# Optimization experiments

Measured on AMD Instinct MI355X. Metric: run time of the kernel, lower is better.

## Reference

```python
import jax, jax.numpy as jnp
import numpy as np

IN_F = 512
OUT_F = 512
TREES = 50
DEPTH = 10  # levels above leaves; 2^DEPTH leaves per tree


def _build_forest(T, D):
    """Forest of T perfect binary trees. Nodes laid out level-by-level (leaves first).
    Returns node_order [N], adjacency [E,2] (parent, child; children consecutive,
    left then right, edges sorted by parent), edge_order [E]."""
    per = 2 ** (D + 1) - 1
    no = np.zeros(per, np.int64)
    adj_parts, eo_parts = [], []
    start, prev = 0, None
    for l in range(D + 1):
        n_l = 2 ** (D - l)
        idx = np.arange(start, start + n_l, dtype=np.int64)
        no[idx] = l
        if l > 0:
            parents = np.repeat(idx, 2)          # each parent twice
            adj_parts.append(np.stack([parents, prev], 1))  # prev = 2*n_l children, pairs consecutive
            eo_parts.append(np.full(2 * n_l, l, np.int64))
        prev, start = idx, start + n_l
    adj = np.concatenate(adj_parts, 0)
    eo = np.concatenate(eo_parts, 0)
    offs = np.arange(T, dtype=np.int64) * per
    node_order = np.tile(no, T)
    adjacency = (adj[None] + offs[:, None, None]).reshape(-1, 2)
    edge_order = np.tile(eo, T)
    return node_order, adjacency, edge_order


def setup_inputs() -> dict:
    key = jax.random.key(0)
    ks = jax.random.split(key, 8)
    no, adj, eo = _build_forest(TREES, DEPTH)
    N = no.shape[0]
    s_in = 1.0 / np.sqrt(IN_F).astype(np.float32)
    s_h = 1.0 / np.sqrt(OUT_F).astype(np.float32)
    return {
        "features": jax.random.normal(ks[0], (N, IN_F), jnp.float32),
        "node_order": jnp.asarray(no),
        "adjacency_list": jnp.asarray(adj),
        "edge_order": jnp.asarray(eo),
        "W_iou_w": jax.random.normal(ks[1], (3 * OUT_F, IN_F), jnp.float32) * s_in,
        "W_iou_b": jax.random.normal(ks[2], (3 * OUT_F,), jnp.float32) * s_in,
        "U_iou_l": jax.random.normal(ks[3], (3 * OUT_F, OUT_F), jnp.float32) * s_h,
        "U_iou_r": jax.random.normal(ks[4], (3 * OUT_F, OUT_F), jnp.float32) * s_h,
        "W_f_w": jax.random.normal(ks[5], (OUT_F, IN_F), jnp.float32) * s_in,
        "W_f_b": jax.random.normal(ks[6], (OUT_F,), jnp.float32) * s_in,
        "U_f_l": jax.random.normal(ks[7], (OUT_F, OUT_F), jnp.float32) * s_h,
        "U_f_r": jax.random.normal(jax.random.fold_in(key, 99), (OUT_F, OUT_F), jnp.float32) * s_h,
    }


def reference(features, node_order, adjacency_list, edge_order,
              W_iou_w, W_iou_b, U_iou_l, U_iou_r, W_f_w, W_f_b, U_f_l, U_f_r):
    # Tree topology is static integer data: hoist it to numpy so per-level index
    # sets are concrete (the original torch code host-syncs the same way).
    no = np.asarray(node_order)
    ao = np.asarray(adjacency_list)
    eo = np.asarray(edge_order)
    N, H = features.shape[0], W_f_w.shape[0]
    h = jnp.zeros((N, H), features.dtype)
    c = jnp.zeros((N, H), features.dtype)
    for l in range(int(no.max()) + 1):
        nodes = jnp.asarray(np.nonzero(no == l)[0])   # parents at this level, sorted
        x = features[nodes]                            # [P, F]
        if l == 0:
            iou = x @ W_iou_w.T + W_iou_b
            i, o, u = jnp.split(iou, 3, axis=1)
            c_new = jax.nn.sigmoid(i) * jnp.tanh(u)
        else:
            e = ao[eo == l]                            # [2P, 2]; children consecutive per parent
            p_rep = jnp.asarray(e[:, 0])               # parent repeated per child
            children = jnp.asarray(e[:, 1])
            ch = h[children]                           # [2P, H]
            cc = c[children]                           # [2P, H]
            iou = (x @ W_iou_w.T + W_iou_b
                   + ch[0::2] @ U_iou_l.T              # left child h
                   + ch[1::2] @ U_iou_r.T)             # right child h
            i, o, u = jnp.split(iou, 3, axis=1)
            wf = features[p_rep] @ W_f_w.T + W_f_b     # [2P, H]
            f_l = jax.nn.sigmoid(wf + ch @ U_f_l.T)
            f_r = jax.nn.sigmoid(wf + ch @ U_f_r.T)
            fc = (f_l + f_r) * cc                      # [2P, H]
            c_new = jax.nn.sigmoid(i) * jnp.tanh(u) + fc.reshape(-1, 2, H).sum(1)
        h_new = jax.nn.sigmoid(o) * jnp.tanh(c_new)
        c = c.at[nodes].set(c_new)
        h = h.at[nodes].set(h_new)
    return h, c
```

## Files before the change

### kernel.cpp

```cpp
#include <hip/hip_runtime.h>
#include <hip/hip_bf16.h>

#define TREES_ 50
#define PER_ 2047
#define NN_ (TREES_ * PER_)
#define NINT_ (TREES_ * 1023)
#define NLEAF_ (TREES_ * 1024)

typedef __attribute__((ext_vector_type(8))) short s8v;
typedef __attribute__((ext_vector_type(4))) float f4v;

__device__ __forceinline__ unsigned short f2bf(float f) {
  union { float f; unsigned u; } v; v.f = f;
  unsigned r = v.u + 0x7FFFu + ((v.u >> 16) & 1u);
  return (unsigned short)(r >> 16);
}
__device__ __forceinline__ float bf2f(unsigned short s) {
  union { unsigned u; float f; } v; v.u = ((unsigned)s) << 16;
  return v.f;
}
__device__ __forceinline__ float sigm(float x) { return 1.f / (1.f + __expf(-x)); }
__device__ __forceinline__ float tanh_s(float x) {
  float ax = fabsf(x);
  float e = __expf(2.f * ax);
  float t = 1.f - 2.f / (e + 1.f);
  return copysignf(t, x);
}
__device__ __forceinline__ f4v fz4() { f4v z; z[0]=0.f; z[1]=0.f; z[2]=0.f; z[3]=0.f; return z; }

#if defined(__has_builtin)
#if __has_builtin(__builtin_amdgcn_global_load_lds)
#define HAS_GLD 1
#endif
#endif
__device__ __forceinline__ void gld16(const void* g, void* l) {
#ifdef HAS_GLD
  __builtin_amdgcn_global_load_lds(
      (const __attribute__((address_space(1))) unsigned int*)g,
      (__attribute__((address_space(3))) unsigned int*)l, 16, 0, 0);
#else
  *(s8v*)l = *(const s8v*)g;
#endif
}

__device__ __forceinline__ int xcd_swz(int bid, int nwg) {
  int q = nwg >> 3, r = nwg & 7, x = bid & 7, pos = bid >> 3;
  int base = (x < r) ? x * (q + 1) : r * (q + 1) + (x - r) * q;
  return base + pos;
}

#define LDS_BYTE(row, c16) ((row) * 128 + (((c16) ^ ((row) & 7)) << 4))

#define MFMA_STEP(Ap, Bp)                                                     \
  _Pragma("unroll") for (int kk = 0; kk < 2; ++kk) {                          \
    s8v af[4], bf_[4];                                                        \
    _Pragma("unroll") for (int i = 0; i < 4; ++i) {                           \
      int R = wr * 64 + i * 16 + lr;                                          \
      af[i] = *(const s8v*)((const char*)(Ap) + LDS_BYTE(R, kk * 4 + lg));    \
    }                                                                         \
    _Pragma("unroll") for (int j = 0; j < 4; ++j) {                           \
      int R = wc * 64 + j * 16 + lr;                                          \
      bf_[j] = *(const s8v*)((const char*)(Bp) + LDS_BYTE(R, kk * 4 + lg));   \
    }                                                                         \
    _Pragma("unroll") for (int i = 0; i < 4; ++i)                             \
      _Pragma("unroll") for (int j = 0; j < 4; ++j)                           \
        acc[i][j] = __builtin_amdgcn_mfma_f32_16x16x32_bf16(af[i], bf_[j],    \
                                                            acc[i][j], 0, 0, 0); \
  }

#define VMCNT8() asm volatile("s_waitcnt vmcnt(8)" ::: "memory")
#define VMCNT0() asm volatile("s_waitcnt vmcnt(0)" ::: "memory")
#define LGKM0()  asm volatile("s_waitcnt lgkmcnt(0)" ::: "memory")
#define SBAR()   __builtin_amdgcn_s_barrier()
#define SCHEDB() __builtin_amdgcn_sched_barrier(0)

#define PIPELINE(STAGEM, NT)                                       \
  STAGEM(0, 0)                                                     \
  STAGEM(1, 64)                                                    \
  {                                                                \
    int cur = 0;                                                   \
    for (int t = 0; t < (NT) - 1; ++t) {                           \
      VMCNT8(); SBAR();                                            \
      __builtin_amdgcn_s_setprio(1);                               \
      MFMA_STEP(AsB + cur * 8192, BsB + cur * 8192)                \
      __builtin_amdgcn_s_setprio(0);                               \
      LGKM0(); SCHEDB(); SBAR();                                   \
      if (t + 2 < (NT)) { STAGEM(cur, (t + 2) * 64) }              \
      cur ^= 1;                                                    \
    }                                                              \
    VMCNT0(); SBAR();                                              \
    MFMA_STEP(AsB + cur * 8192, BsB + cur * 8192)                  \
  }

__global__ __launch_bounds__(256) void feat2bf(const float* __restrict__ feat,
                                               unsigned short* __restrict__ FB) {
  long long i = (long long)blockIdx.x * 256 + threadIdx.x;
  if (i >= (long long)NN_ * 64) return;
  const float* src = feat + i * 8;
  float4 f0 = *(const float4*)src;
  float4 f1 = *(const float4*)(src + 4);
  s8v v;
  v[0] = (short)f2bf(f0.x); v[1] = (short)f2bf(f0.y);
  v[2] = (short)f2bf(f0.z); v[3] = (short)f2bf(f0.w);
  v[4] = (short)f2bf(f1.x); v[5] = (short)f2bf(f1.y);
  v[6] = (short)f2bf(f1.z); v[7] = (short)f2bf(f1.w);
  *(s8v*)(FB + i * 8) = v;
}

__global__ __launch_bounds__(256) void prep_weights(
    const float* __restrict__ Wiou, const float* __restrict__ Ul,
    const float* __restrict__ Ur,  const float* __restrict__ Wf,
    const float* __restrict__ Ufl, const float* __restrict__ Ufr,
    unsigned short* __restrict__ UCAT2, unsigned short* __restrict__ UFLR,
    unsigned short* __restrict__ WFB) {
  int i = blockIdx.x * 256 + threadIdx.x;
  if (i < 1536 * 1536) {
    int r = i / 1536, c = i - r * 1536;
    float v = (c < 512) ? Ul[r * 512 + c]
            : (c < 1024) ? Ur[r * 512 + (c - 512)]
                         : Wiou[r * 512 + (c - 1024)];
    UCAT2[i] = f2bf(v);
  }
  if (i < 1024 * 512) {
    int r = i >> 9, k = i & 511;
    int c = r >> 1, s = r & 1;
    UFLR[i] = f2bf(s ? Ufr[c * 512 + k] : Ufl[c * 512 + k]);
  }
  if (i < 512 * 512) WFB[i] = f2bf(Wf[i]);
}

__global__ __launch_bounds__(256) void pre_mm(
    const unsigned short* __restrict__ FB, const unsigned short* __restrict__ WFB,
    const unsigned short* __restrict__ UCAT2,
    const float* __restrict__ bfb, const float* __restrict__ biou,
    unsigned short* __restrict__ WF, unsigned short* __restrict__ LIOU,
    int nwgW, int nwgL) {
  __shared__ __align__(16) unsigned short AsB[2 * 128 * 64];
  __shared__ __align__(16) unsigned short BsB[2 * 128 * 64];
  const int tid = threadIdx.x;
  const int wid = tid >> 6, lane = tid & 63;
  const int wr = wid >> 1, wc = wid & 1;
  const int lr = lane & 15, lg = lane >> 4;
  f4v acc[4][4];
#pragma unroll
  for (int i = 0; i < 4; ++i)
#pragma unroll
    for (int j = 0; j < 4; ++j) acc[i][j] = fz4();

  const unsigned short* aA[4]; const unsigned short* aB[4];
  int tm, tn;
  const bool isW = (int)blockIdx.x < nwgW;
  if (isW) {
    const int swz = xcd_swz(blockIdx.x, nwgW);
    tn = swz & 3; tm = swz >> 2;
#pragma unroll
    for (int L = 0; L < 4; ++L) {
      int q = L * 256 + tid;
      int row = q >> 3, c16g = (q & 7) ^ (row & 7);
      int m = tm * 128 + row; if (m >= NINT_) m = NINT_ - 1;
      unsigned t = (unsigned)m / 1023u;
      int node = (int)t * 2047 + 1024 + (m - (int)t * 1023);
      aA[L] = FB + (size_t)node * 512 + c16g * 8;
      int n = tn * 128 + row;
      aB[L] = WFB + (size_t)n * 512 + c16g * 8;
    }
  } else {
    const int swz = xcd_swz((int)blockIdx.x - nwgW, nwgL);
    tn = swz % 12; tm = swz / 12;
#pragma unroll
    for (int L = 0; L < 4; ++L) {
      int q = L * 256 + tid;
      int row = q >> 3, c16g = (q & 7) ^ (row & 7);
      int m = tm * 128 + row;
      int node = (m >> 10) * 2047 + (m & 1023);
      aA[L] = FB + (size_t)node * 512 + c16g * 8;
      int n = tn * 128 + row;
      aB[L] = UCAT2 + (size_t)n * 1536 + 1024 + c16g * 8;
    }
  }
#define STAGE_P(bb, kofs)                                         \
  _Pragma("unroll") for (int L = 0; L < 4; ++L) {                 \
    int q = L * 256 + tid;                                        \
    gld16(aA[L] + (kofs), AsB + (bb) * 8192 + q * 8);             \
    gld16(aB[L] + (kofs), BsB + (bb) * 8192 + q * 8);             \
  }
  PIPELINE(STAGE_P, 8)

  if (isW) {
#pragma unroll
    for (int i = 0; i < 4; ++i)
#pragma unroll
      for (int j = 0; j < 4; ++j) {
        int n = tn * 128 + wc * 64 + j * 16 + lr;
        float bias = bfb[n];
#pragma unroll
        for (int r = 0; r < 4; ++r) {
          int m = tm * 128 + wr * 64 + i * 16 + lg * 4 + r;
          if (m < NINT_) WF[(size_t)m * 512 + n] = f2bf(acc[i][j][r] + bias);
        }
      }
  } else {
#pragma unroll
    for (int i = 0; i < 4; ++i)
#pragma unroll
      for (int j = 0; j < 4; ++j) {
        int n = tn * 128 + wc * 64 + j * 16 + lr;
        float bias = biou[n];
#pragma unroll
        for (int r = 0; r < 4; ++r) {
          int m = tm * 128 + wr * 64 + i * 16 + lg * 4 + r;
          LIOU[(size_t)m * 1536 + n] = f2bf(acc[i][j][r] + bias);
        }
      }
  }
}

__global__ __launch_bounds__(256) void leaf_ew(
    const unsigned short* __restrict__ LIOU,
    float* __restrict__ h_out, float* __restrict__ c_out,
    unsigned short* __restrict__ HB) {
  int idx = blockIdx.x * 256 + threadIdx.x;
  int r = idx >> 7;
  int c4 = (idx & 127) << 2;
  int g = (r >> 10) * 2047 + (r & 1023);
  const unsigned short* pr = LIOU + (size_t)r * 1536;
  ushort4 iv = *(const ushort4*)(pr + c4);
  ushort4 ov = *(const ushort4*)(pr + 512 + c4);
  ushort4 uv = *(const ushort4*)(pr + 1024 + c4);
  float4 hv, cv; ushort4 hb;
  float cc, hh;
  cc = sigm(bf2f(iv.x)) * tanh_s(bf2f(uv.x)); hh = sigm(bf2f(ov.x)) * tanh_s(cc);
  cv.x = cc; hv.x = hh; hb.x = f2bf(hh);
  cc = sigm(bf2f(iv.y)) * tanh_s(bf2f(uv.y)); hh = sigm(bf2f(ov.y)) * tanh_s(cc);
  cv.y = cc; hv.y = hh; hb.y = f2bf(hh);
  cc = sigm(bf2f(iv.z)) * tanh_s(bf2f(uv.z)); hh = sigm(bf2f(ov.z)) * tanh_s(cc);
  cv.z = cc; hv.z = hh; hb.z = f2bf(hh);
  cc = sigm(bf2f(iv.w)) * tanh_s(bf2f(uv.w)); hh = sigm(bf2f(ov.w)) * tanh_s(cc);
  cv.w = cc; hv.w = hh; hb.w = f2bf(hh);
  *(float4*)(h_out + (size_t)g * 512 + c4) = hv;
  *(float4*)(c_out + (size_t)g * 512 + c4) = cv;
  *(ushort4*)(HB + (size_t)g * 512 + c4) = hb;
}

__global__ __launch_bounds__(256) void lvl_gemm(
    const unsigned short* __restrict__ HB, const unsigned short* __restrict__ FB,
    const unsigned short* __restrict__ UFLR, const unsigned short* __restrict__ UCAT2,
    const unsigned short* __restrict__ WF, const float* __restrict__ biou,
    const float* __restrict__ c_out, float* __restrict__ h_out,
    unsigned short* __restrict__ IOU,
    int P, int shift, int start_l, int start_lm1, int nwg1, int nwg2) {
  __shared__ __align__(16) unsigned short AsB[2 * 128 * 64];
  __shared__ __align__(16) unsigned short BsB[2 * 128 * 64];
  const int tid = threadIdx.x;
  const int wid = tid >> 6, lane = tid & 63;
  const int wr = wid >> 1, wc = wid & 1;
  const int lr = lane & 15, lg = lane >> 4;
  const int pmask = (1 << shift) - 1;
  f4v acc[4][4];
#pragma unroll
  for (int i = 0; i < 4; ++i)
#pragma unroll
    for (int j = 0; j < 4; ++j) acc[i][j] = fz4();

  if ((int)blockIdx.x < nwg1) {
    const int swz = xcd_swz(blockIdx.x, nwg1);
    const int tn = swz & 7, tm = swz >> 3;
    const int M2 = 2 * P;
    const int cmask = (2 << shift) - 1;
    const unsigned short* aA[4]; const unsigned short* aB[4];
#pragma unroll
    for (int L = 0; L < 4; ++L) {
      int q = L * 256 + tid;
      int row = q >> 3, c16g = (q & 7) ^ (row & 7);
      int jg = tm * 128 + row; if (jg >= M2) jg = M2 - 1;
      int t = jg >> (shift + 1), idx = jg & cmask;
      aA[L] = HB + (size_t)(t * PER_ + start_lm1 + idx) * 512 + c16g * 8;
      int n = tn * 128 + row;
      aB[L] = UFLR + (size_t)n * 512 + c16g * 8;
    }
#define STAGE_G1(bb, kofs)                                        \
  _Pragma("unroll") for (int L = 0; L < 4; ++L) {                 \
    int q = L * 256 + tid;                                        \
    gld16(aA[L] + (kofs), AsB + (bb) * 8192 + q * 8);             \
    gld16(aB[L] + (kofs), BsB + (bb) * 8192 + q * 8);             \
  }
    PIPELINE(STAGE_G1, 8)

    const int soff = start_l - 1024;
#pragma unroll
    for (int i = 0; i < 4; ++i) {
      int mbase = tm * 128 + wr * 64 + i * 16;
#pragma unroll
      for (int j = 0; j < 4; ++j) {
        int nn = tn * 128 + wc * 64 + j * 16 + lr;
        int hcol = nn >> 1;
        float fc[4];
#pragma unroll
        for (int r = 0; r < 4; ++r) {
          int m = mbase + lg * 4 + r;
          int mm = (m < M2) ? m : 0;
          int pidx = mm >> 1;
          int t = pidx >> shift, k = pidx & pmask;
          float wf = bf2f(WF[(size_t)(t * 1023 + soff + k) * 512 + hcol]);
          float sv = sigm(wf + acc[i][j][r]);
          float spair = sv + __shfl_xor(sv, 1, 64);
          float cc = 0.f;
          if ((lr & 1) == 0)
            cc = c_out[(size_t)(t * PER_ + start_lm1 + (mm & cmask)) * 512 + hcol];
          fc[r] = spair * cc;
        }
        if ((lr & 1) == 0) {
          int p0 = (mbase >> 1) + lg * 2;
          if (p0 < P) {
            int t0 = p0 >> shift, k0p = p0 & pmask;
            h_out[(size_t)(t0 * PER_ + start_l + k0p) * 512 + hcol] = fc[0] + fc[1];
          }
          int p1 = (mbase >> 1) + lg * 2 + 1;
          if (p1 < P) {
            int t1 = p1 >> shift, k1p = p1 & pmask;
            h_out[(size_t)(t1 * PER_ + start_l + k1p) * 512 + hcol] = fc[2] + fc[3];
          }
        }
      }
    }
  } else {
    const int swz = xcd_swz((int)blockIdx.x - nwg1, nwg2);
    const int tn = swz % 12, tm = swz / 12;
    const unsigned short* aHB[4]; const unsigned short* aFB[4];
    const unsigned short* aB[4];
#pragma unroll
    for (int L = 0; L < 4; ++L) {
      int q = L * 256 + tid;
      int row = q >> 3, c16g = (q & 7) ^ (row & 7);
      int p = tm * 128 + row; if (p >= P) p = P - 1;
      int t = p >> shift, kp = p & pmask;
      aHB[L] = HB + (size_t)(t * PER_ + start_lm1) * 512 + (size_t)kp * 1024 + c16g * 8;
      aFB[L] = FB + (size_t)(t * PER_ + start_l + kp) * 512 + c16g * 8 - 1024;
      int n = tn * 128 + row;
      aB[L] = UCAT2 + (size_t)n * 1536 + c16g * 8;
    }
#define STAGE_G2(bb, kofs)                                                    \
  _Pragma("unroll") for (int L = 0; L < 4; ++L) {                             \
    int q = L * 256 + tid;                                                    \
    const unsigned short* srcA =                                              \
        ((kofs) < 1024) ? aHB[L] + (kofs) : aFB[L] + (kofs);                  \
    gld16(srcA, AsB + (bb) * 8192 + q * 8);                                   \
    gld16(aB[L] + (kofs), BsB + (bb) * 8192 + q * 8);                         \
  }
    PIPELINE(STAGE_G2, 24)
#pragma unroll
    for (int i = 0; i < 4; ++i)
#pragma unroll
      for (int j = 0; j < 4; ++j) {
        int n = tn * 128 + wc * 64 + j * 16 + lr;
        float bias = biou[n];
#pragma unroll
        for (int r = 0; r < 4; ++r) {
          int m = tm * 128 + wr * 64 + i * 16 + lg * 4 + r;
          if (m < P) IOU[(size_t)m * 1536 + n] = f2bf(acc[i][j][r] + bias);
        }
      }
  }
}

__global__ __launch_bounds__(256) void g3_kernel(
    const unsigned short* __restrict__ IOU,
    float* __restrict__ h_out, float* __restrict__ c_out,
    unsigned short* __restrict__ HB, int P, int shift, int start_l) {
  int idx = blockIdx.x * 256 + threadIdx.x;
  int p = idx >> 7;
  if (p >= P) return;
  int c4 = (idx & 127) << 2;
  int t = p >> shift, k = p & ((1 << shift) - 1);
  size_t pg = (size_t)(t * PER_ + start_l + k);
  const unsigned short* ir = IOU + (size_t)p * 1536;
  ushort4 iv = *(const ushort4*)(ir + c4);
  ushort4 ov = *(const ushort4*)(ir + 512 + c4);
  ushort4 uv = *(const ushort4*)(ir + 1024 + c4);
  float4 fcs = *(const float4*)(h_out + pg * 512 + c4);
  float4 hv, cv; ushort4 hb;
  float cc, hh;
  cc = sigm(bf2f(iv.x)) * tanh_s(bf2f(uv.x)) + fcs.x; hh = sigm(bf2f(ov.x)) * tanh_s(cc);
  cv.x = cc; hv.x = hh; hb.x = f2bf(hh);
  cc = sigm(bf2f(iv.y)) * tanh_s(bf2f(uv.y)) + fcs.y; hh = sigm(bf2f(ov.y)) * tanh_s(cc);
  cv.y = cc; hv.y = hh; hb.y = f2bf(hh);
  cc = sigm(bf2f(iv.z)) * tanh_s(bf2f(uv.z)) + fcs.z; hh = sigm(bf2f(ov.z)) * tanh_s(cc);
  cv.z = cc; hv.z = hh; hb.z = f2bf(hh);
  cc = sigm(bf2f(iv.w)) * tanh_s(bf2f(uv.w)) + fcs.w; hh = sigm(bf2f(ov.w)) * tanh_s(cc);
  cv.w = cc; hv.w = hh; hb.w = f2bf(hh);
  *(float4*)(h_out + pg * 512 + c4) = hv;
  *(float4*)(c_out + pg * 512 + c4) = cv;
  *(ushort4*)(HB + pg * 512 + c4) = hb;
}

__global__ void fill_sentinel(float* out, int n) {
  int i = blockIdx.x * 256 + threadIdx.x;
  if (i < n) out[i] = 12345.0f;
}

extern "C" void kernel_launch(void* const* d_in, const int* in_sizes, int n_in,
                              void* d_out, int out_size, void* d_ws, size_t ws_size,
                              hipStream_t stream) {
  (void)in_sizes; (void)n_in; (void)out_size;
  const float* feat = (const float*)d_in[0];
  const float* Wiou = (const float*)d_in[4];
  const float* biou = (const float*)d_in[5];
  const float* Ul   = (const float*)d_in[6];
  const float* Ur   = (const float*)d_in[7];
  const float* Wf   = (const float*)d_in[8];
  const float* bfb  = (const float*)d_in[9];
  const float* Ufl  = (const float*)d_in[10];
  const float* Ufr  = (const float*)d_in[11];
  float* h_out = (float*)d_out;
  float* c_out = h_out + (size_t)NN_ * 512;

  const size_t OFF_HB   = 0;
  const size_t SZ_HB    = (size_t)NN_ * 512 * 2;
  const size_t OFF_FB   = OFF_HB + SZ_HB;
  const size_t SZ_FB    = (size_t)NN_ * 512 * 2;
  const size_t OFF_WFm  = OFF_FB + SZ_FB;
  const size_t SZ_WF    = (size_t)NINT_ * 512 * 2;
  const size_t OFF_UC2  = OFF_WFm + SZ_WF;
  const size_t SZ_UC2   = 1536 * 1536 * 2;
  const size_t OFF_UFLR = OFF_UC2 + SZ_UC2;
  const size_t SZ_UFLR  = 1024 * 512 * 2;
  const size_t OFF_WFB  = OFF_UFLR + SZ_UFLR;
  const size_t SZ_WFB   = 512 * 512 * 2;
  const size_t OFF_LIOU = OFF_WFB + SZ_WFB;
  const size_t SZ_LIOU  = (size_t)NLEAF_ * 1536 * 2;
  const size_t NEEDED   = OFF_LIOU + SZ_LIOU;

  if (ws_size < NEEDED) {
    int n = 2 * NN_ * 512;
    fill_sentinel<<<(n + 255) / 256, 256, 0, stream>>>((float*)d_out, n);
    return;
  }

  char* ws = (char*)d_ws;
  unsigned short* HB    = (unsigned short*)(ws + OFF_HB);
  unsigned short* FB    = (unsigned short*)(ws + OFF_FB);
  unsigned short* WF    = (unsigned short*)(ws + OFF_WFm);
  unsigned short* UCAT2 = (unsigned short*)(ws + OFF_UC2);
  unsigned short* UFLR  = (unsigned short*)(ws + OFF_UFLR);
  unsigned short* WFB   = (unsigned short*)(ws + OFF_WFB);
  unsigned short* LIOU  = (unsigned short*)(ws + OFF_LIOU);
  unsigned short* IOU   = (unsigned short*)(ws + OFF_LIOU);

  prep_weights<<<9216, 256, 0, stream>>>(Wiou, Ul, Ur, Wf, Ufl, Ufr,
                                         UCAT2, UFLR, WFB);
  feat2bf<<<(NN_ * 64 + 255) / 256, 256, 0, stream>>>(feat, FB);
  {
    int nwgW = ((NINT_ + 127) / 128) * 4;
    int nwgL = (NLEAF_ / 128) * 12;
    pre_mm<<<nwgW + nwgL, 256, 0, stream>>>(FB, WFB, UCAT2, bfb, biou,
                                            WF, LIOU, nwgW, nwgL);
  }
  leaf_ew<<<(NLEAF_ * 128) / 256, 256, 0, stream>>>(LIOU, h_out, c_out, HB);

  for (int l = 1; l <= 10; ++l) {
    int shift = 10 - l;
    int P = TREES_ << shift;
    int start_l   = 2048 - (1 << (11 - l));
    int start_lm1 = 2048 - (1 << (12 - l));
    int nwg1 = ((2 * P + 127) / 128) * 8;
    int nwg2 = ((P + 127) / 128) * 12;
    lvl_gemm<<<nwg1 + nwg2, 256, 0, stream>>>(HB, FB, UFLR, UCAT2, WF, biou,
                                              c_out, h_out, IOU,
                                              P, shift, start_l, start_lm1,
                                              nwg1, nwg2);
    int g3b = (P * 128 + 255) / 256;
    g3_kernel<<<g3b, 256, 0, stream>>>(IOU, h_out, c_out, HB, P, shift, start_l);
  }
}
```

Measured before the change: 1.460 ms.

## Split fused GEMM kernels and retile IOU GEMM with 256-wide triple-buffered tiles

Splits the merged pre-GEMM into separate wf_gemm and pre_mm launches, and splits the per-level fused kernel into g1_kernel (forget gates) and g2_kernel (IOU). g2 now uses 512-thread blocks with 128x256 tiles and a three-stage LDS ring with a wait of vmcnt(6), aiming for more B-tile reuse and deeper load/compute overlap. The cost is extra launches per level, and the forget and IOU GEMMs, which were independent, now run one after the other instead of concurrently.

Result: slower. 1.788 ms (+22.5%).

```diff
diff --git a/kernel.cpp b/kernel.cpp
--- a/kernel.cpp
+++ b/kernel.cpp
@@ -69,6 +69,7 @@
   }
 
 #define VMCNT8() asm volatile("s_waitcnt vmcnt(8)" ::: "memory")
+#define VMCNT6() asm volatile("s_waitcnt vmcnt(6)" ::: "memory")
 #define VMCNT0() asm volatile("s_waitcnt vmcnt(0)" ::: "memory")
 #define LGKM0()  asm volatile("s_waitcnt lgkmcnt(0)" ::: "memory")
 #define SBAR()   __builtin_amdgcn_s_barrier()
@@ -129,12 +130,60 @@
   if (i < 512 * 512) WFB[i] = f2bf(Wf[i]);
 }
 
+__global__ __launch_bounds__(256) void wf_gemm(
+    const unsigned short* __restrict__ FB, const unsigned short* __restrict__ WFB,
+    const float* __restrict__ bfb, unsigned short* __restrict__ WF, int nwg) {
+  __shared__ __align__(16) unsigned short AsB[2 * 128 * 64];
+  __shared__ __align__(16) unsigned short BsB[2 * 128 * 64];
+  const int tid = threadIdx.x;
+  const int swz = xcd_swz(blockIdx.x, nwg);
+  const int tn = swz & 3, tm = swz >> 2;
+  const int wid = tid >> 6, lane = tid & 63;
+  const int wr = wid >> 1, wc = wid & 1;
+  const int lr = lane & 15, lg = lane >> 4;
+  const unsigned short* aA[4]; const unsigned short* aB[4];
+#pragma unroll
+  for (int L = 0; L < 4; ++L) {
+    int q = L * 256 + tid;
+    int row = q >> 3, c16g = (q & 7) ^ (row & 7);
+    int m = tm * 128 + row; if (m >= NINT_) m = NINT_ - 1;
+    int t = (int)((unsigned)m / 1023u);
+    int node = t * 2047 + 1024 + (m - t * 1023);
+    aA[L] = FB + (size_t)node * 512 + c16g * 8;
+    int n = tn * 128 + row;
+    aB[L] = WFB + (size_t)n * 512 + c16g * 8;
+  }
+  f4v acc[4][4];
+#pragma unroll
+  for (int i = 0; i < 4; ++i)
+#pragma unroll
+    for (int j = 0; j < 4; ++j) acc[i][j] = fz4();
+#define STAGE_W(bb, kofs)                                         \
+  _Pragma("unroll") for (int L = 0; L < 4; ++L) {                 \
+    int q = L * 256 + tid;                                        \
+    gld16(aA[L] + (kofs), AsB + (bb) * 8192 + q * 8);             \
+    gld16(aB[L] + (kofs), BsB + (bb) * 8192 + q * 8);             \
+  }
+  PIPELINE(STAGE_W, 8)
+#pragma unroll
+  for (int i = 0; i < 4; ++i)
+#pragma unroll
+    for (int j = 0; j < 4; ++j) {
+      int n = tn * 128 + wc * 64 + j * 16 + lr;
+      float bias = bfb[n];
+#pragma unroll
+      for (int r = 0; r < 4; ++r) {
+        int m = tm * 128 + wr * 64 + i * 16 + lg * 4 + r;
+        if (m < NINT_) WF[(size_t)m * 512 + n] = f2bf(acc[i][j][r] + bias);
+      }
+    }
+}
+
 __global__ __launch_bounds__(256) void pre_mm(
-    const unsigned short* __restrict__ FB, const unsigned short* __restrict__ WFB,
+    const unsigned short* __restrict__ FB,
     const unsigned short* __restrict__ UCAT2,
-    const float* __restrict__ bfb, const float* __restrict__ biou,
-    unsigned short* __restrict__ WF, unsigned short* __restrict__ LIOU,
-    int nwgW, int nwgL) {
+    const float* __restrict__ biou,
+    unsigned short* __restrict__ LIOU, int nwg) {
   __shared__ __align__(16) unsigned short AsB[2 * 128 * 64];
   __shared__ __align__(16) unsigned short BsB[2 * 128 * 64];
   const int tid = threadIdx.x;
@@ -146,37 +195,18 @@
   for (int i = 0; i < 4; ++i)
 #pragma unroll
     for (int j = 0; j < 4; ++j) acc[i][j] = fz4();
-
   const unsigned short* aA[4]; const unsigned short* aB[4];
-  int tm, tn;
-  const bool isW = (int)blockIdx.x < nwgW;
-  if (isW) {
-    const int swz = xcd_swz(blockIdx.x, nwgW);
-    tn = swz & 3; tm = swz >> 2;
-#pragma unroll
-    for (int L = 0; L < 4; ++L) {
-      int q = L * 256 + tid;
-      int row = q >> 3, c16g = (q & 7) ^ (row & 7);
-      int m = tm * 128 + row; if (m >= NINT_) m = NINT_ - 1;
-      unsigned t = (unsigned)m / 1023u;
-      int node = (int)t * 2047 + 1024 + (m - (int)t * 1023);
-      aA[L] = FB + (size_t)node * 512 + c16g * 8;
-      int n = tn * 128 + row;
-      aB[L] = WFB + (size_t)n * 512 + c16g * 8;
-    }
-  } else {
-    const int swz = xcd_swz((int)blockIdx.x - nwgW, nwgL);
-    tn = swz % 12; tm = swz / 12;
-#pragma unroll
-    for (int L = 0; L < 4; ++L) {
-      int q = L * 256 + tid;
-      int row = q >> 3, c16g = (q & 7) ^ (row & 7);
-      int m = tm * 128 + row;
-      int node = (m >> 10) * 2047 + (m & 1023);
-      aA[L] = FB + (size_t)node * 512 + c16g * 8;
-      int n = tn * 128 + row;
-      aB[L] = UCAT2 + (size_t)n * 1536 + 1024 + c16g * 8;
-    }
+  const int swz = xcd_swz(blockIdx.x, nwg);
+  const int tn = swz % 12, tm = swz / 12;
+#pragma unroll
+  for (int L = 0; L < 4; ++L) {
+    int q = L * 256 + tid;
+    int row = q >> 3, c16g = (q & 7) ^ (row & 7);
+    int m = tm * 128 + row;
+    int node = (m >> 10) * 2047 + (m & 1023);
+    aA[L] = FB + (size_t)node * 512 + c16g * 8;
+    int n = tn * 128 + row;
+    aB[L] = UCAT2 + (size_t)n * 1536 + 1024 + c16g * 8;
   }
 #define STAGE_P(bb, kofs)                                         \
   _Pragma("unroll") for (int L = 0; L < 4; ++L) {                 \
@@ -185,34 +215,18 @@
     gld16(aB[L] + (kofs), BsB + (bb) * 8192 + q * 8);             \
   }
   PIPELINE(STAGE_P, 8)
-
-  if (isW) {
-#pragma unroll
-    for (int i = 0; i < 4; ++i)
-#pragma unroll
-      for (int j = 0; j < 4; ++j) {
-        int n = tn * 128 + wc * 64 + j * 16 + lr;
-        float bias = bfb[n];
-#pragma unroll
-        for (int r = 0; r < 4; ++r) {
-          int m = tm * 128 + wr * 64 + i * 16 + lg * 4 + r;
-          if (m < NINT_) WF[(size_t)m * 512 + n] = f2bf(acc[i][j][r] + bias);
-        }
+#pragma unroll
+  for (int i = 0; i < 4; ++i)
+#pragma unroll
+    for (int j = 0; j < 4; ++j) {
+      int n = tn * 128 + wc * 64 + j * 16 + lr;
+      float bias = biou[n];
+#pragma unroll
+      for (int r = 0; r < 4; ++r) {
+        int m = tm * 128 + wr * 64 + i * 16 + lg * 4 + r;
+        LIOU[(size_t)m * 1536 + n] = f2bf(acc[i][j][r] + bias);
       }
-  } else {
-#pragma unroll
-    for (int i = 0; i < 4; ++i)
-#pragma unroll
-      for (int j = 0; j < 4; ++j) {
-        int n = tn * 128 + wc * 64 + j * 16 + lr;
-        float bias = biou[n];
-#pragma unroll
-        for (int r = 0; r < 4; ++r) {
-          int m = tm * 128 + wr * 64 + i * 16 + lg * 4 + r;
-          LIOU[(size_t)m * 1536 + n] = f2bf(acc[i][j][r] + bias);
-        }
-      }
-  }
+    }
 }
 
 __global__ __launch_bounds__(256) void leaf_ew(
@@ -242,13 +256,11 @@
   *(ushort4*)(HB + (size_t)g * 512 + c4) = hb;
 }
 
-__global__ __launch_bounds__(256) void lvl_gemm(
-    const unsigned short* __restrict__ HB, const unsigned short* __restrict__ FB,
-    const unsigned short* __restrict__ UFLR, const unsigned short* __restrict__ UCAT2,
-    const unsigned short* __restrict__ WF, const float* __restrict__ biou,
-    const float* __restrict__ c_out, float* __restrict__ h_out,
-    unsigned short* __restrict__ IOU,
-    int P, int shift, int start_l, int start_lm1, int nwg1, int nwg2) {
+__global__ __launch_bounds__(256) void g1_kernel(
+    const unsigned short* __restrict__ HB, const unsigned short* __restrict__ UFLR,
+    const unsigned short* __restrict__ WF, const float* __restrict__ c_out,
+    float* __restrict__ h_out,
+    int P, int shift, int start_l, int start_lm1, int nwg) {
   __shared__ __align__(16) unsigned short AsB[2 * 128 * 64];
   __shared__ __align__(16) unsigned short BsB[2 * 128 * 64];
   const int tid = threadIdx.x;
@@ -256,111 +268,168 @@
   const int wr = wid >> 1, wc = wid & 1;
   const int lr = lane & 15, lg = lane >> 4;
   const int pmask = (1 << shift) - 1;
+  const int swz = xcd_swz(blockIdx.x, nwg);
+  const int tn = swz & 7, tm = swz >> 3;
+  const int M2 = 2 * P;
+  const int cmask = (2 << shift) - 1;
   f4v acc[4][4];
 #pragma unroll
   for (int i = 0; i < 4; ++i)
 #pragma unroll
     for (int j = 0; j < 4; ++j) acc[i][j] = fz4();
-
-  if ((int)blockIdx.x < nwg1) {
-    const int swz = xcd_swz(blockIdx.x, nwg1);
-    const int tn = swz & 7, tm = swz >> 3;
-    const int M2 = 2 * P;
-    const int cmask = (2 << shift) - 1;
-    const unsigned short* aA[4]; const unsigned short* aB[4];
-#pragma unroll
-    for (int L = 0; L < 4; ++L) {
-      int q = L * 256 + tid;
-      int row = q >> 3, c16g = (q & 7) ^ (row & 7);
-      int jg = tm * 128 + row; if (jg >= M2) jg = M2 - 1;
-      int t = jg >> (shift + 1), idx = jg & cmask;
-      aA[L] = HB + (size_t)(t * PER_ + start_lm1 + idx) * 512 + c16g * 8;
-      int n = tn * 128 + row;
-      aB[L] = UFLR + (size_t)n * 512 + c16g * 8;
-    }
+  const unsigned short* aA[4]; const unsigned short* aB[4];
+#pragma unroll
+  for (int L = 0; L < 4; ++L) {
+    int q = L * 256 + tid;
+    int row = q >> 3, c16g = (q & 7) ^ (row & 7);
+    int jg = tm * 128 + row; if (jg >= M2) jg = M2 - 1;
+    int t = jg >> (shift + 1), idx = jg & cmask;
+    aA[L] = HB + (size_t)(t * PER_ + start_lm1 + idx) * 512 + c16g * 8;
+    int n = tn * 128 + row;
+    aB[L] = UFLR + (size_t)n * 512 + c16g * 8;
+  }
 #define STAGE_G1(bb, kofs)                                        \
   _Pragma("unroll") for (int L = 0; L < 4; ++L) {                 \
     int q = L * 256 + tid;                                        \
     gld16(aA[L] + (kofs), AsB + (bb) * 8192 + q * 8);             \
     gld16(aB[L] + (kofs), BsB + (bb) * 8192 + q * 8);             \
   }
-    PIPELINE(STAGE_G1, 8)
-
-    const int soff = start_l - 1024;
-#pragma unroll
-    for (int i = 0; i < 4; ++i) {
-      int mbase = tm * 128 + wr * 64 + i * 16;
-#pragma unroll
-      for (int j = 0; j < 4; ++j) {
-        int nn = tn * 128 + wc * 64 + j * 16 + lr;
-        int hcol = nn >> 1;
-        float fc[4];
-#pragma unroll
-        for (int r = 0; r < 4; ++r) {
-          int m = mbase + lg * 4 + r;
-          int mm = (m < M2) ? m : 0;
-          int pidx = mm >> 1;
-          int t = pidx >> shift, k = pidx & pmask;
-          float wf = bf2f(WF[(size_t)(t * 1023 + soff + k) * 512 + hcol]);
-          float sv = sigm(wf + acc[i][j][r]);
-          float spair = sv + __shfl_xor(sv, 1, 64);
-          float cc = 0.f;
-          if ((lr & 1) == 0)
-            cc = c_out[(size_t)(t * PER_ + start_lm1 + (mm & cmask)) * 512 + hcol];
-          fc[r] = spair * cc;
+  PIPELINE(STAGE_G1, 8)
+
+  const int soff = start_l - 1024;
+#pragma unroll
+  for (int i = 0; i < 4; ++i) {
+    int mbase = tm * 128 + wr * 64 + i * 16;
+#pragma unroll
+    for (int j = 0; j < 4; ++j) {
+      int nn = tn * 128 + wc * 64 + j * 16 + lr;
+      int hcol = nn >> 1;
+      float fc[4];
+#pragma unroll
+      for (int r = 0; r < 4; ++r) {
+        int m = mbase + lg * 4 + r;
+        int mm = (m < M2) ? m : 0;
+        int pidx = mm >> 1;
+        int t = pidx >> shift, k = pidx & pmask;
+        float wf = bf2f(WF[(size_t)(t * 1023 + soff + k) * 512 + hcol]);
+        float sv = sigm(wf + acc[i][j][r]);
+        float spair = sv + __shfl_xor(sv, 1, 64);
+        float cc = 0.f;
+        if ((lr & 1) == 0)
+          cc = c_out[(size_t)(t * PER_ + start_lm1 + (mm & cmask)) * 512 + hcol];
+        fc[r] = spair * cc;
+      }
+      if ((lr & 1) == 0) {
+        int p0 = (mbase >> 1) + lg * 2;
+        if (p0 < P) {
+          int t0 = p0 >> shift, k0p = p0 & pmask;
+          h_out[(size_t)(t0 * PER_ + start_l + k0p) * 512 + hcol] = fc[0] + fc[1];
         }
-        if ((lr & 1) == 0) {
-          int p0 = (mbase >> 1) + lg * 2;
-          if (p0 < P) {
-            int t0 = p0 >> shift, k0p = p0 & pmask;
-            h_out[(size_t)(t0 * PER_ + start_l + k0p) * 512 + hcol] = fc[0] + fc[1];
-          }
-          int p1 = (mbase >> 1) + lg * 2 + 1;
-          if (p1 < P) {
-            int t1 = p1 >> shift, k1p = p1 & pmask;
-            h_out[(size_t)(t1 * PER_ + start_l + k1p) * 512 + hcol] = fc[2] + fc[3];
-          }
+        int p1 = (mbase >> 1) + lg * 2 + 1;
+        if (p1 < P) {
+          int t1 = p1 >> shift, k1p = p1 & pmask;
+          h_out[(size_t)(t1 * PER_ + start_l + k1p) * 512 + hcol] = fc[2] + fc[3];
         }
       }
     }
-  } else {
-    const int swz = xcd_swz((int)blockIdx.x - nwg1, nwg2);
-    const int tn = swz % 12, tm = swz / 12;
-    const unsigned short* aHB[4]; const unsigned short* aFB[4];
-    const unsigned short* aB[4];
-#pragma unroll
-    for (int L = 0; L < 4; ++L) {
-      int q = L * 256 + tid;
-      int row = q >> 3, c16g = (q & 7) ^ (row & 7);
-      int p = tm * 128 + row; if (p >= P) p = P - 1;
-      int t = p >> shift, kp = p & pmask;
-      aHB[L] = HB + (size_t)(t * PER_ + start_lm1) * 512 + (size_t)kp * 1024 + c16g * 8;
-      aFB[L] = FB + (size_t)(t * PER_ + start_l + kp) * 512 + c16g * 8 - 1024;
-      int n = tn * 128 + row;
-      aB[L] = UCAT2 + (size_t)n * 1536 + c16g * 8;
-    }
-#define STAGE_G2(bb, kofs)                                                    \
-  _Pragma("unroll") for (int L = 0; L < 4; ++L) {                             \
-    int q = L * 256 + tid;                                                    \
+  }
+}
+
+__global__ __launch_bounds__(512, 2) void g2_kernel(
+    const unsigned short* __restrict__ HB, const unsigned short* __restrict__ FB,
+    const unsigned short* __restrict__ UCAT2, const float* __restrict__ biou,
+    unsigned short* __restrict__ IOU,
+    int P, int shift, int start_l, int start_lm1, int nwg) {
+  __shared__ __align__(16) unsigned short AsR[3 * 128 * 64];
+  __shared__ __align__(16) unsigned short BsR[3 * 256 * 64];
+  const int tid = threadIdx.x;
+  const int wid = tid >> 6, lane = tid & 63;
+  const int wm = wid >> 2, wn = wid & 3;
+  const int lr = lane & 15, lg = lane >> 4;
+  const int pmask = (1 << shift) - 1;
+  const int rowt = tid >> 3;
+  const int c16g = (tid & 7) ^ (rowt & 7);
+  const int swz = xcd_swz(blockIdx.x, nwg);
+  const int tn = swz % 6, tm = swz / 6;
+
+  f4v acc[4][4];
+#pragma unroll
+  for (int i = 0; i < 4; ++i)
+#pragma unroll
+    for (int j = 0; j < 4; ++j) acc[i][j] = fz4();
+
+  const unsigned short* aHB[2]; const unsigned short* aFB[2];
+#pragma unroll
+  for (int L = 0; L < 2; ++L) {
+    int row = L * 64 + rowt;
+    int p = tm * 128 + row; if (p >= P) p = P - 1;
+    int t = p >> shift, kp = p & pmask;
+    aHB[L] = HB + (size_t)(t * PER_ + start_lm1) * 512 + (size_t)kp * 1024 + c16g * 8;
+    aFB[L] = FB + (size_t)(t * PER_ + start_l + kp) * 512 + c16g * 8 - 1024;
+  }
+  const unsigned short* aB0 =
+      UCAT2 + (size_t)(tn * 256 + rowt) * 1536 + c16g * 8;
+
+#define STAGE_G2(slot, kofs)                                                  \
+  _Pragma("unroll") for (int L = 0; L < 2; ++L) {                             \
     const unsigned short* srcA =                                              \
         ((kofs) < 1024) ? aHB[L] + (kofs) : aFB[L] + (kofs);                  \
-    gld16(srcA, AsB + (bb) * 8192 + q * 8);                                   \
-    gld16(aB[L] + (kofs), BsB + (bb) * 8192 + q * 8);                         \
-  }
-    PIPELINE(STAGE_G2, 24)
-#pragma unroll
-    for (int i = 0; i < 4; ++i)
-#pragma unroll
-      for (int j = 0; j < 4; ++j) {
-        int n = tn * 128 + wc * 64 + j * 16 + lr;
-        float bias = biou[n];
-#pragma unroll
-        for (int r = 0; r < 4; ++r) {
-          int m = tm * 128 + wr * 64 + i * 16 + lg * 4 + r;
-          if (m < P) IOU[(size_t)m * 1536 + n] = f2bf(acc[i][j][r] + bias);
-        }
+    gld16(srcA, AsR + (slot) * 8192 + (L * 512 + tid) * 8);                   \
+  }                                                                           \
+  _Pragma("unroll") for (int L = 0; L < 4; ++L) {                             \
+    gld16(aB0 + (size_t)L * 64 * 1536 + (kofs),                               \
+          BsR + (slot) * 16384 + (L * 512 + tid) * 8);                        \
+  }
+#define MFMA_G2(slot)                                                         \
+  _Pragma("unroll") for (int kk = 0; kk < 2; ++kk) {                          \
+    s8v af[4], bf_[4];                                                        \
+    _Pragma("unroll") for (int i = 0; i < 4; ++i) {                           \
+      int R = wm * 64 + i * 16 + lr;                                          \
+      af[i] = *(const s8v*)((const char*)(AsR + (slot) * 8192) +              \
+                            LDS_BYTE(R, kk * 4 + lg));                        \
+    }                                                                         \
+    _Pragma("unroll") for (int j = 0; j < 4; ++j) {                           \
+      int R = wn * 64 + j * 16 + lr;                                          \
+      bf_[j] = *(const s8v*)((const char*)(BsR + (slot) * 16384) +            \
+                             LDS_BYTE(R, kk * 4 + lg));                       \
+    }                                                                         \
+    _Pragma("unroll") for (int i = 0; i < 4; ++i)                             \
+      _Pragma("unroll") for (int j = 0; j < 4; ++j)                           \
+        acc[i][j] = __builtin_amdgcn_mfma_f32_16x16x32_bf16(af[i], bf_[j],    \
+                                                            acc[i][j], 0, 0, 0); \
+  }
+
+  STAGE_G2(0, 0)
+  STAGE_G2(1, 64)
+  const int NT = 24;
+  int t = 0;
+  for (; t < NT - 1; ++t) {
+    VMCNT6(); SBAR();
+    int s = t % 3;
+    if (t + 2 < NT) {
+      int s2 = (t + 2) % 3;
+      STAGE_G2(s2, (t + 2) * 64)
+    }
+    __builtin_amdgcn_s_setprio(1);
+    MFMA_G2(s)
+    __builtin_amdgcn_s_setprio(0);
+    LGKM0(); SCHEDB(); SBAR();
+  }
+  VMCNT0(); SBAR();
+  MFMA_G2(t % 3)
+
+#pragma unroll
+  for (int i = 0; i < 4; ++i)
+#pragma unroll
+    for (int j = 0; j < 4; ++j) {
+      int n = tn * 256 + wn * 64 + j * 16 + lr;
+      float bias = biou[n];
+#pragma unroll
+      for (int r = 0; r < 4; ++r) {
+        int m = tm * 128 + wm * 64 + i * 16 + lg * 4 + r;
+        if (m < P) IOU[(size_t)m * 1536 + n] = f2bf(acc[i][j][r] + bias);
       }
-  }
+    }
 }
 
 __global__ __launch_bounds__(256) void g3_kernel(
@@ -451,9 +520,11 @@
   feat2bf<<<(NN_ * 64 + 255) / 256, 256, 0, stream>>>(feat, FB);
   {
     int nwgW = ((NINT_ + 127) / 128) * 4;
+    wf_gemm<<<nwgW, 256, 0, stream>>>(FB, WFB, bfb, WF, nwgW);
+  }
+  {
     int nwgL = (NLEAF_ / 128) * 12;
-    pre_mm<<<nwgW + nwgL, 256, 0, stream>>>(FB, WFB, UCAT2, bfb, biou,
-                                            WF, LIOU, nwgW, nwgL);
+    pre_mm<<<nwgL, 256, 0, stream>>>(FB, UCAT2, biou, LIOU, nwgL);
   }
   leaf_ew<<<(NLEAF_ * 128) / 256, 256, 0, stream>>>(LIOU, h_out, c_out, HB);
 
@@ -463,11 +534,11 @@
     int start_l   = 2048 - (1 << (11 - l));
     int start_lm1 = 2048 - (1 << (12 - l));
     int nwg1 = ((2 * P + 127) / 128) * 8;
-    int nwg2 = ((P + 127) / 128) * 12;
-    lvl_gemm<<<nwg1 + nwg2, 256, 0, stream>>>(HB, FB, UFLR, UCAT2, WF, biou,
-                                              c_out, h_out, IOU,
-                                              P, shift, start_l, start_lm1,
-                                              nwg1, nwg2);
+    g1_kernel<<<nwg1, 256, 0, stream>>>(HB, UFLR, WF, c_out, h_out,
+                                        P, shift, start_l, start_lm1, nwg1);
+    int nwg2 = ((P + 127) / 128) * 6;
+    g2_kernel<<<nwg2, 512, 0, stream>>>(HB, FB, UCAT2, biou, IOU,
+                                        P, shift, start_l, start_lm1, nwg2);
     int g3b = (P * 128 + 255) / 256;
     g3_kernel<<<g3b, 256, 0, stream>>>(IOU, h_out, c_out, HB, P, shift, start_l);
   }
```
